# Kernel tuning notes

Hardware: AMD Instinct MI355X
Metric: run time of the kernel (lower is better)

Reference implementation:

```python
import jax, jax.numpy as jnp
import numpy as np

OUT_H, OUT_W = 7, 7

def _bin_bounds(n, bins):
    # Mirrors ops.linspace(0, n, bins+1) with floor(start) / min(ceil(end), n)
    idx = np.linspace(0.0, float(n), bins + 1)
    starts = np.floor(idx[:-1]).astype(np.int64)
    ends = np.minimum(np.ceil(idx[1:]).astype(np.int64), n)
    return starts, ends


def setup_inputs() -> dict:
    key = jax.random.key(0)
    x = jax.random.normal(key, (16, 224, 224, 128), dtype=jnp.float32)
    return {"x": x}


def reference(x):
    # Adaptive average pooling 2D, channels_last (B, H, W, C) -> (B, OUT_H, OUT_W, C).
    B, H, W, C = x.shape
    hs, he = _bin_bounds(H, OUT_H)
    ws, we = _bin_bounds(W, OUT_W)
    rows = []
    for i in range(OUT_H):
        cols = []
        for j in range(OUT_W):
            region = x[:, hs[i]:he[i], ws[j]:we[j], :]  # (B, bh, bw, C), static slice
            cols.append(jnp.mean(region, axis=(1, 2), keepdims=True))
        rows.append(jnp.concatenate(cols, axis=2))
    return jnp.concatenate(rows, axis=1)
```

## Files before the change

### kernel.cpp

```cpp
#include <hip/hip_runtime.h>
#include <hip/hip_bf16.h>


#define REGIONS (16 * 7 * 7)

__global__ __launch_bounds__(256) void AdaptivePooling2D_48146583388556_kernel(
    const float* __restrict__ x, float* __restrict__ out) {
    const int bid = blockIdx.x;
    const int t   = threadIdx.x;

    const int b   = bid / 49;
    const int rem = bid - b * 49;
    const int i   = rem / 7;
    const int j   = rem - i * 7;

    const size_t base_f = ((size_t)(b * 224 + i * 32) * 224 + (size_t)j * 32) * 128;
    const float4* base = reinterpret_cast<const float4*>(x + base_f);
    const size_t row_stride4 = (size_t)224 * 128 / 4;

    float4 acc = make_float4(0.f, 0.f, 0.f, 0.f);
    #pragma unroll 4
    for (int h = 0; h < 32; ++h) {
        const float4* row = base + (size_t)h * row_stride4;
        #pragma unroll
        for (int k = 0; k < 4; ++k) {
            float4 v = row[k * 256 + t];
            acc.x += v.x; acc.y += v.y; acc.z += v.z; acc.w += v.w;
        }
    }

    __shared__ float4 sm[256];
    sm[t] = acc;
    __syncthreads();

    if (t < 32) {
        float4 s = sm[t];
        #pragma unroll
        for (int k = 1; k < 8; ++k) {
            float4 v = sm[t + 32 * k];
            s.x += v.x; s.y += v.y; s.z += v.z; s.w += v.w;
        }
        const float scale = 1.0f / 1024.0f;
        float4 o = make_float4(s.x * scale, s.y * scale, s.z * scale, s.w * scale);
        reinterpret_cast<float4*>(out + (size_t)bid * 128)[t] = o;
    }
}

extern "C" void kernel_launch(void* const* d_in, const int* in_sizes, int n_in,
                              void* d_out, int out_size, void* d_ws, size_t ws_size,
                              hipStream_t stream) {
    const float* x  = (const float*)d_in[0];
    float* out      = (float*)d_out;
    AdaptivePooling2D_48146583388556_kernel<<<REGIONS, 256, 0, stream>>>(x, out);
}
```

Measured before the change: 82.36 us.

## Split each pooling region across row chunks with a second reduce pass

Each 32x32 pooling region is split into 8 (or 4) row chunks handled by separate blocks, which write partial sums to workspace; a second small kernel sums the partials and scales. This raises the grid from 784 blocks to 6272 so more CUs stay busy streaming the 411 MB input. In exchange it adds a second launch and a workspace round trip, and it falls back to the original single-pass kernel when the workspace is too small.

Result: faster. 79.55 us (-3.4%).

```diff
diff --git a/kernel.cpp b/kernel.cpp
--- a/kernel.cpp
+++ b/kernel.cpp
@@ -3,24 +3,30 @@
 
 
 #define REGIONS (16 * 7 * 7)
+#define OUT_ELEMS (REGIONS * 128)
 
-__global__ __launch_bounds__(256) void AdaptivePooling2D_48146583388556_kernel(
-    const float* __restrict__ x, float* __restrict__ out) {
+template <int CHUNKS>
+__global__ __launch_bounds__(256) void pool_partial(const float* __restrict__ x,
+                                                    float* __restrict__ ws) {
+    constexpr int ROWS = 32 / CHUNKS;
     const int bid = blockIdx.x;
     const int t   = threadIdx.x;
 
-    const int b   = bid / 49;
-    const int rem = bid - b * 49;
+    const int region = bid / CHUNKS;
+    const int chunk  = bid - region * CHUNKS;
+    const int b   = region / 49;
+    const int rem = region - b * 49;
     const int i   = rem / 7;
     const int j   = rem - i * 7;
 
-    const size_t base_f = ((size_t)(b * 224 + i * 32) * 224 + (size_t)j * 32) * 128;
+    const size_t base_f =
+        ((size_t)(b * 224 + i * 32 + chunk * ROWS) * 224 + (size_t)j * 32) * 128;
     const float4* base = reinterpret_cast<const float4*>(x + base_f);
     const size_t row_stride4 = (size_t)224 * 128 / 4;
 
     float4 acc = make_float4(0.f, 0.f, 0.f, 0.f);
-    #pragma unroll 4
-    for (int h = 0; h < 32; ++h) {
+    #pragma unroll
+    for (int h = 0; h < ROWS; ++h) {
         const float4* row = base + (size_t)h * row_stride4;
         #pragma unroll
         for (int k = 0; k < 4; ++k) {
@@ -40,6 +46,54 @@
             float4 v = sm[t + 32 * k];
             s.x += v.x; s.y += v.y; s.z += v.z; s.w += v.w;
         }
+        reinterpret_cast<float4*>(ws + (size_t)bid * 128)[t] = s;
+    }
+}
+
+template <int CHUNKS>
+__global__ __launch_bounds__(256) void pool_reduce(const float* __restrict__ ws,
+                                                   float* __restrict__ out) {
+    const int e = blockIdx.x * 256 + threadIdx.x;
+    const int r  = e >> 7;
+    const int ch = e & 127;
+    float s = 0.f;
+    #pragma unroll
+    for (int c = 0; c < CHUNKS; ++c)
+        s += ws[(size_t)(r * CHUNKS + c) * 128 + ch];
+    out[e] = s * (1.0f / 1024.0f);
+}
+
+__global__ __launch_bounds__(256) void pool_direct(const float* __restrict__ x,
+                                                   float* __restrict__ out) {
+    const int bid = blockIdx.x;
+    const int t   = threadIdx.x;
+    const int b   = bid / 49;
+    const int rem = bid - b * 49;
+    const int i   = rem / 7;
+    const int j   = rem - i * 7;
+    const size_t base_f = ((size_t)(b * 224 + i * 32) * 224 + (size_t)j * 32) * 128;
+    const float4* base = reinterpret_cast<const float4*>(x + base_f);
+    const size_t row_stride4 = (size_t)224 * 128 / 4;
+    float4 acc = make_float4(0.f, 0.f, 0.f, 0.f);
+    #pragma unroll 4
+    for (int h = 0; h < 32; ++h) {
+        const float4* row = base + (size_t)h * row_stride4;
+        #pragma unroll
+        for (int k = 0; k < 4; ++k) {
+            float4 v = row[k * 256 + t];
+            acc.x += v.x; acc.y += v.y; acc.z += v.z; acc.w += v.w;
+        }
+    }
+    __shared__ float4 sm[256];
+    sm[t] = acc;
+    __syncthreads();
+    if (t < 32) {
+        float4 s = sm[t];
+        #pragma unroll
+        for (int k = 1; k < 8; ++k) {
+            float4 v = sm[t + 32 * k];
+            s.x += v.x; s.y += v.y; s.z += v.z; s.w += v.w;
+        }
         const float scale = 1.0f / 1024.0f;
         float4 o = make_float4(s.x * scale, s.y * scale, s.z * scale, s.w * scale);
         reinterpret_cast<float4*>(out + (size_t)bid * 128)[t] = o;
@@ -49,7 +103,20 @@
 extern "C" void kernel_launch(void* const* d_in, const int* in_sizes, int n_in,
                               void* d_out, int out_size, void* d_ws, size_t ws_size,
                               hipStream_t stream) {
-    const float* x  = (const float*)d_in[0];
-    float* out      = (float*)d_out;
-    AdaptivePooling2D_48146583388556_kernel<<<REGIONS, 256, 0, stream>>>(x, out);
+    const float* x = (const float*)d_in[0];
+    float* out     = (float*)d_out;
+    float* ws      = (float*)d_ws;
+
+    constexpr size_t need8 = (size_t)REGIONS * 8 * 128 * sizeof(float);
+    constexpr size_t need4 = (size_t)REGIONS * 4 * 128 * sizeof(float);
+
+    if (ws_size >= need8) {
+        pool_partial<8><<<REGIONS * 8, 256, 0, stream>>>(x, ws);
+        pool_reduce<8><<<OUT_ELEMS / 256, 256, 0, stream>>>(ws, out);
+    } else if (ws_size >= need4) {
+        pool_partial<4><<<REGIONS * 4, 256, 0, stream>>>(x, ws);
+        pool_reduce<4><<<OUT_ELEMS / 256, 256, 0, stream>>>(ws, out);
+    } else {
+        pool_direct<<<REGIONS, 256, 0, stream>>>(x, out);
+    }
 }
```

## Split pooling into per-row-pair partial sums plus a second reduction kernel

Applied to the files above, without the earlier changes.

Replaces the one-block-per-output-region kernel with a two-stage scheme. Each of 1792 blocks sums two full image rows into seven column-bin partials and writes them to workspace, and a second kernel sums the 16 row-pair partials per bin and scales. The aim is more parallel blocks, contiguous streaming reads and more loads in flight, at the cost of an extra launch and workspace traffic. The original kernel is kept as a fallback when the workspace is too small.

Result: no change. 81.56 us (-1.0%).

```diff
diff --git a/kernel.cpp b/kernel.cpp
--- a/kernel.cpp
+++ b/kernel.cpp
@@ -2,37 +2,101 @@
 #include <hip/hip_bf16.h>
 
 
-#define REGIONS (16 * 7 * 7)
+#define NROWBLK 1792
+#define WS_F4_PER_BLK 224
 
-__global__ __launch_bounds__(256) void AdaptivePooling2D_48146583388556_kernel(
-    const float* __restrict__ x, float* __restrict__ out) {
+__global__ __launch_bounds__(256) void pool_rows(const float* __restrict__ x,
+                                                 float* __restrict__ ws) {
+    const int r = blockIdx.x;
+    const int t = threadIdx.x;
+    const int wv = t >> 6;
+    const int lane = t & 63;
+
+    const float4* base = reinterpret_cast<const float4*>(x) + (size_t)r * 2 * 7168;
+
+    float4 acc[7];
+    #pragma unroll
+    for (int j = 0; j < 7; ++j) acc[j] = make_float4(0.f, 0.f, 0.f, 0.f);
+
+    #pragma unroll
+    for (int row = 0; row < 2; ++row) {
+        const float4* p = base + row * 7168;
+        #pragma unroll
+        for (int k = 0; k < 28; ++k) {
+            float4 v = p[k * 256 + t];
+            const int j = k >> 2;
+            acc[j].x += v.x; acc[j].y += v.y; acc[j].z += v.z; acc[j].w += v.w;
+        }
+    }
+
+    #pragma unroll
+    for (int j = 0; j < 7; ++j) {
+        acc[j].x += __shfl_xor(acc[j].x, 32);
+        acc[j].y += __shfl_xor(acc[j].y, 32);
+        acc[j].z += __shfl_xor(acc[j].z, 32);
+        acc[j].w += __shfl_xor(acc[j].w, 32);
+    }
+
+    __shared__ float4 sm[7][128];
+    if (lane < 32) {
+        #pragma unroll
+        for (int j = 0; j < 7; ++j) sm[j][wv * 32 + lane] = acc[j];
+    }
+    __syncthreads();
+
+    if (t < WS_F4_PER_BLK) {
+        const int j = t >> 5, g = t & 31;
+        float4 s = sm[j][g];
+        #pragma unroll
+        for (int w = 1; w < 4; ++w) {
+            float4 v = sm[j][w * 32 + g];
+            s.x += v.x; s.y += v.y; s.z += v.z; s.w += v.w;
+        }
+        reinterpret_cast<float4*>(ws)[(size_t)r * WS_F4_PER_BLK + t] = s;
+    }
+}
+
+__global__ __launch_bounds__(256) void pool_reduce_rows(const float* __restrict__ ws,
+                                                        float* __restrict__ out) {
+    const int e4 = blockIdx.x * 256 + threadIdx.x;
+    const int g  = e4 & 31;
+    const int j  = (e4 >> 5) % 7;
+    const int bi = (e4 >> 5) / 7;
+    const float4* w4 = reinterpret_cast<const float4*>(ws);
+    float4 s = make_float4(0.f, 0.f, 0.f, 0.f);
+    #pragma unroll
+    for (int c = 0; c < 16; ++c) {
+        float4 v = w4[(size_t)(bi * 16 + c) * WS_F4_PER_BLK + j * 32 + g];
+        s.x += v.x; s.y += v.y; s.z += v.z; s.w += v.w;
+    }
+    const float sc = 1.0f / 1024.0f;
+    float4 o = make_float4(s.x * sc, s.y * sc, s.z * sc, s.w * sc);
+    reinterpret_cast<float4*>(out)[e4] = o;
+}
+
+__global__ __launch_bounds__(256) void pool_direct(const float* __restrict__ x,
+                                                   float* __restrict__ out) {
     const int bid = blockIdx.x;
     const int t   = threadIdx.x;
-
     const int b   = bid / 49;
     const int rem = bid - b * 49;
     const int i   = rem / 7;
     const int j   = rem - i * 7;
-
     const size_t base_f = ((size_t)(b * 224 + i * 32) * 224 + (size_t)j * 32) * 128;
     const float4* base = reinterpret_cast<const float4*>(x + base_f);
-    const size_t row_stride4 = (size_t)224 * 128 / 4;
-
     float4 acc = make_float4(0.f, 0.f, 0.f, 0.f);
     #pragma unroll 4
     for (int h = 0; h < 32; ++h) {
-        const float4* row = base + (size_t)h * row_stride4;
+        const float4* row = base + (size_t)h * 7168;
         #pragma unroll
         for (int k = 0; k < 4; ++k) {
             float4 v = row[k * 256 + t];
             acc.x += v.x; acc.y += v.y; acc.z += v.z; acc.w += v.w;
         }
     }
-
     __shared__ float4 sm[256];
     sm[t] = acc;
     __syncthreads();
-
     if (t < 32) {
         float4 s = sm[t];
         #pragma unroll
@@ -40,8 +104,8 @@
             float4 v = sm[t + 32 * k];
             s.x += v.x; s.y += v.y; s.z += v.z; s.w += v.w;
         }
-        const float scale = 1.0f / 1024.0f;
-        float4 o = make_float4(s.x * scale, s.y * scale, s.z * scale, s.w * scale);
+        const float sc = 1.0f / 1024.0f;
+        float4 o = make_float4(s.x * sc, s.y * sc, s.z * sc, s.w * sc);
         reinterpret_cast<float4*>(out + (size_t)bid * 128)[t] = o;
     }
 }
@@ -49,7 +113,15 @@
 extern "C" void kernel_launch(void* const* d_in, const int* in_sizes, int n_in,
                               void* d_out, int out_size, void* d_ws, size_t ws_size,
                               hipStream_t stream) {
-    const float* x  = (const float*)d_in[0];
-    float* out      = (float*)d_out;
-    AdaptivePooling2D_48146583388556_kernel<<<REGIONS, 256, 0, stream>>>(x, out);
+    const float* x = (const float*)d_in[0];
+    float* out     = (float*)d_out;
+    float* ws      = (float*)d_ws;
+
+    constexpr size_t need = (size_t)NROWBLK * WS_F4_PER_BLK * sizeof(float4);
+    if (ws_size >= need) {
+        pool_rows<<<NROWBLK, 256, 0, stream>>>(x, ws);
+        pool_reduce_rows<<<25088 / 256, 256, 0, stream>>>(ws, out);
+    } else {
+        pool_direct<<<16 * 7 * 7, 256, 0, stream>>>(x, out);
+    }
 }
```
